# Performance work log

Measured on AMD Instinct MI355X. Metric: run time of the kernel, lower is better.

## Reference

```python
import jax, jax.numpy as jnp
import numpy as np

A, B, N, FEAT, H, R, E_PER, NACT = 3, 4096, 64, 32, 32, 6, 1536, 16


def setup_inputs() -> dict:
    key = jax.random.key(0)
    ks = jax.random.split(key, 12)
    s = 0.1
    return {
        "unary": jax.random.normal(ks[0], (A, B, N, FEAT), jnp.float32),
        "actions": jax.random.normal(ks[1], (A, B, NACT), jnp.float32),
        "w_rel": jax.random.normal(ks[2], (R, FEAT, H), jnp.float32) * s,
        "w_root": jax.random.normal(ks[3], (FEAT, H), jnp.float32) * s,
        "b_gnn": jax.random.normal(ks[4], (H,), jnp.float32) * s,
        "w1": jax.random.normal(ks[5], (A, H + NACT * (A - 1), H), jnp.float32) * s,
        "b1": jax.random.normal(ks[6], (A, H), jnp.float32) * s,
        "w2": jax.random.normal(ks[7], (A, H, NACT), jnp.float32) * s,
        "b2": jax.random.normal(ks[8], (A, NACT), jnp.float32) * s,
        "edge_src": jax.random.randint(ks[9], (E_PER,), 0, N, jnp.int32),
        "edge_dst": jax.random.randint(ks[10], (E_PER,), 0, N, jnp.int32),
        "edge_rel": jax.random.randint(ks[11], (E_PER,), 0, R, jnp.int32),
    }


def reference(unary, actions, w_rel, w_root, b_gnn, w1, b1, w2, b2,
              edge_src, edge_dst, edge_rel):
    NT = B * N  # total nodes in the batched graph
    # Replicate the shared per-graph edge list across the batch with node offsets
    offs = (jnp.arange(B, dtype=jnp.int32) * N)[:, None]
    src = (edge_src[None, :] + offs).reshape(-1)            # [E]
    dst = (edge_dst[None, :] + offs).reshape(-1)            # [E]
    rel = jnp.tile(edge_rel, B)                             # [E]
    seg = dst * R + rel                                     # per (node, relation) segment
    cnt = jax.ops.segment_sum(jnp.ones_like(rel, jnp.float32), seg,
                              num_segments=NT * R)
    inv_deg = 1.0 / jnp.maximum(cnt, 1.0)                   # RGCN mean per relation
    norm_e = inv_deg[seg][:, None]

    def rgcn_relu(x):  # x: [NT, FEAT]
        h_stack = jnp.einsum('ni,rio->rno', x, w_rel)       # [R, NT, H]
        msg = h_stack[rel, src] * norm_e                    # [E, H] gather-transform
        agg = jax.ops.segment_sum(msg, dst, num_segments=NT)
        return jax.nn.relu(agg + x @ w_root + b_gnn)

    qs = []
    for a in range(A):
        h = rgcn_relu(unary[a].reshape(NT, FEAT))           # [NT, H]
        pooled = h.reshape(B, N, H).max(axis=1)             # global max pool per graph
        others = jnp.concatenate([actions[j] for j in range(A) if j != a], axis=1)
        critic_in = jnp.concatenate([pooled, others], axis=1)
        mid = jax.nn.leaky_relu(critic_in @ w1[a] + b1[a], negative_slope=0.01)
        all_q = mid @ w2[a] + b2[a]                         # [B, NACT]
        idx = jnp.argmax(actions[a], axis=1)[:, None]
        qs.append(jnp.take_along_axis(all_q, idx, axis=1))  # [B, 1]
    return jnp.stack(qs)                                    # [A, B, 1]
```

## Files before the change

### kernel.cpp

```cpp
#include <hip/hip_runtime.h>
#include <hip/hip_bf16.h>
#include <math.h>

#define A_AG   3
#define Bq     4096
#define Nn     64
#define FEAT   32
#define Hh     32
#define Rr     6
#define E_PER  1536
#define NACT   16

#define KCAT    224
#define XSTRIDE 232
#define TSTRIDE 72
#define NDR     384
#define NEXT    448

typedef __attribute__((ext_vector_type(8))) short          bfrag;
typedef __attribute__((ext_vector_type(4))) float          f32x4;
typedef __attribute__((ext_vector_type(8))) unsigned short u16x8;

__device__ __forceinline__ ushort f2bf(float x) {
    unsigned u = __float_as_uint(x);
    u = (u + 0x7fffu + ((u >> 16) & 1u)) >> 16;
    return (ushort)u;
}
__device__ __forceinline__ float bf2f(ushort b) {
    return __uint_as_float(((unsigned)b) << 16);
}
__device__ __forceinline__ unsigned cvt_pk_bf16(float lo, float hi) {
    unsigned r;
    asm volatile("v_cvt_pk_bf16_f32 %0, %1, %2" : "=v"(r) : "v"(lo), "v"(hi));
    return r;
}

__global__ __launch_bounds__(1024) void prep(
        const float* __restrict__ w_rel,
        const float* __restrict__ w_root,
        const int* __restrict__ esrc,
        const int* __restrict__ edst,
        const int* __restrict__ erel,
        float*  __restrict__ Adjf,
        ushort* __restrict__ Adjbf,
        ushort* __restrict__ Wt_g) {
    __shared__ int   cnt[NDR];
    __shared__ float invd[NEXT];
    const int t = threadIdx.x;

    for (int i = t; i < NDR; i += 1024) cnt[i] = 0;
    __syncthreads();
    for (int e = t; e < E_PER; e += 1024)
        atomicAdd(&cnt[edst[e] * Rr + erel[e]], 1);
    __syncthreads();
    for (int i = t; i < NEXT; i += 1024)
        invd[i] = (i < NDR) ? 1.0f / fmaxf((float)cnt[i], 1.0f) : 1.0f;
    for (int i = t; i < NEXT * Nn; i += 1024) Adjf[i] = 0.f;
    __syncthreads();
    for (int e = t; e < E_PER; e += 1024)
        atomicAdd(&Adjf[(edst[e] * Rr + erel[e]) * Nn + esrc[e]], 1.0f);
    if (t < Nn) Adjf[(NDR + t) * Nn + t] = 1.0f;
    __syncthreads();
    for (int i = t; i < NEXT * Nn; i += 1024)
        Adjbf[i] = f2bf(Adjf[i] * invd[i >> 6]);
    for (int i = t; i < Hh * KCAT; i += 1024) {
        const int h = i / KCAT, kk = i % KCAT;
        float v;
        if (kk < 192) v = w_rel[(((kk >> 5) * FEAT) + (kk & 31)) * Hh + h];
        else          v = w_root[(kk - 192) * Hh + h];
        Wt_g[i] = f2bf(v);
    }
}

__global__ __launch_bounds__(256, 4) void critic_kernel(
    const float* __restrict__ unary,
    const float* __restrict__ actions,
    const float* __restrict__ b_gnn,
    const float* __restrict__ w1,
    const float* __restrict__ b1,
    const float* __restrict__ w2,
    const float* __restrict__ b2,
    const ushort* __restrict__ Adj,
    const ushort* __restrict__ Wt,
    float* __restrict__ out)
{
    const int b = blockIdx.x;
    const int a = blockIdx.y;
    const int t = threadIdx.x;

    __shared__ ushort Xt[FEAT * TSTRIDE];
    __shared__ ushort xcat[Nn * XSTRIDE];
    __shared__ float pmax[4][32];
    __shared__ float cin[64];
    __shared__ float mid[32];
    __shared__ float allq[16];

    {
        const int f = t & 31, sg = t >> 5;
        const float* xp = unary + ((((size_t)a * Bq + b) * Nn + sg * 8) * FEAT) + f;
        unsigned w0 = cvt_pk_bf16(xp[0 * FEAT], xp[1 * FEAT]);
        unsigned w1_ = cvt_pk_bf16(xp[2 * FEAT], xp[3 * FEAT]);
        unsigned w2_ = cvt_pk_bf16(xp[4 * FEAT], xp[5 * FEAT]);
        unsigned w3 = cvt_pk_bf16(xp[6 * FEAT], xp[7 * FEAT]);
        uint4 v = {w0, w1_, w2_, w3};
        *(uint4*)&Xt[f * TSTRIDE + sg * 8] = v;
    }
    __syncthreads();

    {
        const int l = t & 63, w = t >> 6;
        const int lr = l & 15, kg = l >> 4;

        bfrag af[2][2];
        #pragma unroll
        for (int mt = 0; mt < 2; ++mt)
            #pragma unroll
            for (int ks = 0; ks < 2; ++ks)
                af[mt][ks] = *(const bfrag*)&Xt[(mt * 16 + lr) * TSTRIDE + ks * 32 + kg * 8];

        const ushort* abase = Adj + (size_t)(w * 7 * 16 + lr) * Nn + kg * 8;
        f32x4 acc[7][2];
        #pragma unroll
        for (int i = 0; i < 7; ++i) {
            acc[i][0] = (f32x4){0.f, 0.f, 0.f, 0.f};
            acc[i][1] = (f32x4){0.f, 0.f, 0.f, 0.f};
        }
        #pragma unroll
        for (int i = 0; i < 7; ++i) {
            const bfrag b0 = *(const bfrag*)(abase + i * 16 * Nn);
            const bfrag b1f = *(const bfrag*)(abase + i * 16 * Nn + 32);
            acc[i][0] = __builtin_amdgcn_mfma_f32_16x16x32_bf16(af[0][0], b0,  acc[i][0], 0, 0, 0);
            acc[i][1] = __builtin_amdgcn_mfma_f32_16x16x32_bf16(af[1][0], b0,  acc[i][1], 0, 0, 0);
            acc[i][0] = __builtin_amdgcn_mfma_f32_16x16x32_bf16(af[0][1], b1f, acc[i][0], 0, 0, 0);
            acc[i][1] = __builtin_amdgcn_mfma_f32_16x16x32_bf16(af[1][1], b1f, acc[i][1], 0, 0, 0);
        }
        #pragma unroll
        for (int i = 0; i < 7; ++i) {
            const int nt = w * 7 + i;
            const int dr = nt * 16 + lr;
            int row, colb;
            if (nt < 24) {
                const int d = (dr * 10923) >> 16;
                const int r = dr - 6 * d;
                row = d; colb = r * 32;
            } else {
                row = dr - NDR; colb = 192;
            }
            #pragma unroll
            for (int mt = 0; mt < 2; ++mt) {
                const unsigned lo = cvt_pk_bf16(acc[i][mt][0], acc[i][mt][1]);
                const unsigned hi = cvt_pk_bf16(acc[i][mt][2], acc[i][mt][3]);
                uint2 v = {lo, hi};
                *(uint2*)&xcat[row * XSTRIDE + colb + mt * 16 + kg * 4] = v;
            }
        }
    }
    __syncthreads();

    {
        const int l = t & 63, w = t >> 6;
        const int lr = l & 15, kg = l >> 4;
        const ushort* arow  = &xcat[(w * 16 + lr) * XSTRIDE + kg * 8];
        const ushort* bcol0 = Wt + lr * KCAT + kg * 8;
        const ushort* bcol1 = Wt + (16 + lr) * KCAT + kg * 8;
        f32x4 acc0 = {0.f, 0.f, 0.f, 0.f};
        f32x4 acc1 = {0.f, 0.f, 0.f, 0.f};
        #pragma unroll
        for (int ks = 0; ks < 7; ++ks) {
            const bfrag afr = *(const bfrag*)(arow + ks * 32);
            const bfrag b0  = *(const bfrag*)(bcol0 + ks * 32);
            const bfrag b1  = *(const bfrag*)(bcol1 + ks * 32);
            acc0 = __builtin_amdgcn_mfma_f32_16x16x32_bf16(afr, b0, acc0, 0, 0, 0);
            acc1 = __builtin_amdgcn_mfma_f32_16x16x32_bf16(afr, b1, acc1, 0, 0, 0);
        }
        const float bg0 = b_gnn[lr], bg1 = b_gnn[16 + lr];
        float m0 = -INFINITY, m1 = -INFINITY;
        #pragma unroll
        for (int j = 0; j < 4; ++j) {
            m0 = fmaxf(m0, fmaxf(acc0[j] + bg0, 0.f));
            m1 = fmaxf(m1, fmaxf(acc1[j] + bg1, 0.f));
        }
        m0 = fmaxf(m0, __shfl_xor(m0, 16));
        m0 = fmaxf(m0, __shfl_xor(m0, 32));
        m1 = fmaxf(m1, __shfl_xor(m1, 16));
        m1 = fmaxf(m1, __shfl_xor(m1, 32));
        if (l < 16) { pmax[w][lr] = m0; pmax[w][16 + lr] = m1; }
    }
    __syncthreads();

    if (t < 32) {
        cin[t] = fmaxf(fmaxf(pmax[0][t], pmax[1][t]),
                       fmaxf(pmax[2][t], pmax[3][t]));
    } else if (t < 64) {
        const int k   = t - 32;
        const int jj  = k >> 4;
        const int col = k & 15;
        const int other = (jj == 0) ? (a == 0 ? 1 : 0) : (a == 2 ? 1 : 2);
        cin[t] = actions[((size_t)other * Bq + b) * NACT + col];
    }
    __syncthreads();

    if (t < 32) {
        float acc = b1[a * Hh + t];
        #pragma unroll
        for (int k = 0; k < 64; ++k)
            acc = fmaf(cin[k], w1[((size_t)a * 64 + k) * Hh + t], acc);
        mid[t] = acc > 0.f ? acc : 0.01f * acc;
    }
    __syncthreads();

    if (t < 16) {
        float acc = b2[a * NACT + t];
        #pragma unroll
        for (int k = 0; k < 32; ++k)
            acc = fmaf(mid[k], w2[((size_t)a * Hh + k) * NACT + t], acc);
        allq[t] = acc;
    }
    __syncthreads();

    if (t == 0) {
        const float* act = actions + ((size_t)a * Bq + b) * NACT;
        int best = 0;
        float bv = act[0];
        #pragma unroll
        for (int j = 1; j < NACT; ++j) {
            float v = act[j];
            if (v > bv) { bv = v; best = j; }
        }
        out[(size_t)a * Bq + b] = allq[best];
    }
}

extern "C" void kernel_launch(void* const* d_in, const int* in_sizes, int n_in,
                              void* d_out, int out_size, void* d_ws, size_t ws_size,
                              hipStream_t stream) {
    const float* unary   = (const float*)d_in[0];
    const float* actions = (const float*)d_in[1];
    const float* w_rel   = (const float*)d_in[2];
    const float* w_root  = (const float*)d_in[3];
    const float* b_gnn   = (const float*)d_in[4];
    const float* w1      = (const float*)d_in[5];
    const float* b1      = (const float*)d_in[6];
    const float* w2      = (const float*)d_in[7];
    const float* b2      = (const float*)d_in[8];
    const int* edge_src  = (const int*)d_in[9];
    const int* edge_dst  = (const int*)d_in[10];
    const int* edge_rel  = (const int*)d_in[11];
    float* out = (float*)d_out;

    char* ws = (char*)d_ws;
    ushort* Adjbf = (ushort*)(ws + 0);
    ushort* Wt_g  = (ushort*)(ws + 57344);
    float*  Adjf  = (float*)(ws + 71680);

    prep<<<1, 1024, 0, stream>>>(w_rel, w_root, edge_src, edge_dst, edge_rel,
                                 Adjf, Adjbf, Wt_g);

    dim3 grid(Bq, A_AG);
    critic_kernel<<<grid, 256, 0, stream>>>(unary, actions, b_gnn,
                                            w1, b1, w2, b2,
                                            Adjbf, Wt_g, out);
}
```

Measured before the change: 302.4 us.

## Split critic MLP tail into separate batched kernel over 8 graphs per block

Moves the pooled-feature MLP head (two small dense layers plus action argmax selection) out of the per-graph GNN kernel into a new tail kernel. The GNN kernel now writes pooled features to workspace, and the tail kernel processes 8 graphs per block with w1/w2 staged in shared memory. This removes serialized tail phases in which most threads sat idle behind several block-wide barriers in every GNN block. The cost is an extra kernel launch and a workspace round trip for the pooled features.

After: 289.5 us. -4.3%, faster.

```diff
diff --git a/kernel.cpp b/kernel.cpp
--- a/kernel.cpp
+++ b/kernel.cpp
@@ -16,18 +16,15 @@
 #define TSTRIDE 72
 #define NDR     384
 #define NEXT    448
+#define GT      8
 
 typedef __attribute__((ext_vector_type(8))) short          bfrag;
 typedef __attribute__((ext_vector_type(4))) float          f32x4;
-typedef __attribute__((ext_vector_type(8))) unsigned short u16x8;
 
 __device__ __forceinline__ ushort f2bf(float x) {
     unsigned u = __float_as_uint(x);
     u = (u + 0x7fffu + ((u >> 16) & 1u)) >> 16;
     return (ushort)u;
-}
-__device__ __forceinline__ float bf2f(ushort b) {
-    return __uint_as_float(((unsigned)b) << 16);
 }
 __device__ __forceinline__ unsigned cvt_pk_bf16(float lo, float hi) {
     unsigned r;
@@ -74,15 +71,10 @@
 
 __global__ __launch_bounds__(256, 4) void critic_kernel(
     const float* __restrict__ unary,
-    const float* __restrict__ actions,
     const float* __restrict__ b_gnn,
-    const float* __restrict__ w1,
-    const float* __restrict__ b1,
-    const float* __restrict__ w2,
-    const float* __restrict__ b2,
     const ushort* __restrict__ Adj,
     const ushort* __restrict__ Wt,
-    float* __restrict__ out)
+    float* __restrict__ pooled_g)
 {
     const int b = blockIdx.x;
     const int a = blockIdx.y;
@@ -91,9 +83,6 @@
     __shared__ ushort Xt[FEAT * TSTRIDE];
     __shared__ ushort xcat[Nn * XSTRIDE];
     __shared__ float pmax[4][32];
-    __shared__ float cin[64];
-    __shared__ float mid[32];
-    __shared__ float allq[16];
 
     {
         const int f = t & 31, sg = t >> 5;
@@ -127,12 +116,12 @@
         }
         #pragma unroll
         for (int i = 0; i < 7; ++i) {
-            const bfrag b0 = *(const bfrag*)(abase + i * 16 * Nn);
-            const bfrag b1f = *(const bfrag*)(abase + i * 16 * Nn + 32);
-            acc[i][0] = __builtin_amdgcn_mfma_f32_16x16x32_bf16(af[0][0], b0,  acc[i][0], 0, 0, 0);
-            acc[i][1] = __builtin_amdgcn_mfma_f32_16x16x32_bf16(af[1][0], b0,  acc[i][1], 0, 0, 0);
-            acc[i][0] = __builtin_amdgcn_mfma_f32_16x16x32_bf16(af[0][1], b1f, acc[i][0], 0, 0, 0);
-            acc[i][1] = __builtin_amdgcn_mfma_f32_16x16x32_bf16(af[1][1], b1f, acc[i][1], 0, 0, 0);
+            const bfrag bb0 = *(const bfrag*)(abase + i * 16 * Nn);
+            const bfrag bb1 = *(const bfrag*)(abase + i * 16 * Nn + 32);
+            acc[i][0] = __builtin_amdgcn_mfma_f32_16x16x32_bf16(af[0][0], bb0, acc[i][0], 0, 0, 0);
+            acc[i][1] = __builtin_amdgcn_mfma_f32_16x16x32_bf16(af[1][0], bb0, acc[i][1], 0, 0, 0);
+            acc[i][0] = __builtin_amdgcn_mfma_f32_16x16x32_bf16(af[0][1], bb1, acc[i][0], 0, 0, 0);
+            acc[i][1] = __builtin_amdgcn_mfma_f32_16x16x32_bf16(af[1][1], bb1, acc[i][1], 0, 0, 0);
         }
         #pragma unroll
         for (int i = 0; i < 7; ++i) {
@@ -168,10 +157,10 @@
         #pragma unroll
         for (int ks = 0; ks < 7; ++ks) {
             const bfrag afr = *(const bfrag*)(arow + ks * 32);
-            const bfrag b0  = *(const bfrag*)(bcol0 + ks * 32);
-            const bfrag b1  = *(const bfrag*)(bcol1 + ks * 32);
-            acc0 = __builtin_amdgcn_mfma_f32_16x16x32_bf16(afr, b0, acc0, 0, 0, 0);
-            acc1 = __builtin_amdgcn_mfma_f32_16x16x32_bf16(afr, b1, acc1, 0, 0, 0);
+            const bfrag bf0 = *(const bfrag*)(bcol0 + ks * 32);
+            const bfrag bf1 = *(const bfrag*)(bcol1 + ks * 32);
+            acc0 = __builtin_amdgcn_mfma_f32_16x16x32_bf16(afr, bf0, acc0, 0, 0, 0);
+            acc1 = __builtin_amdgcn_mfma_f32_16x16x32_bf16(afr, bf1, acc1, 0, 0, 0);
         }
         const float bg0 = b_gnn[lr], bg1 = b_gnn[16 + lr];
         float m0 = -INFINITY, m1 = -INFINITY;
@@ -189,45 +178,86 @@
     __syncthreads();
 
     if (t < 32) {
-        cin[t] = fmaxf(fmaxf(pmax[0][t], pmax[1][t]),
-                       fmaxf(pmax[2][t], pmax[3][t]));
-    } else if (t < 64) {
-        const int k   = t - 32;
-        const int jj  = k >> 4;
-        const int col = k & 15;
-        const int other = (jj == 0) ? (a == 0 ? 1 : 0) : (a == 2 ? 1 : 2);
-        cin[t] = actions[((size_t)other * Bq + b) * NACT + col];
-    }
-    __syncthreads();
-
-    if (t < 32) {
-        float acc = b1[a * Hh + t];
-        #pragma unroll
-        for (int k = 0; k < 64; ++k)
-            acc = fmaf(cin[k], w1[((size_t)a * 64 + k) * Hh + t], acc);
-        mid[t] = acc > 0.f ? acc : 0.01f * acc;
-    }
-    __syncthreads();
-
-    if (t < 16) {
-        float acc = b2[a * NACT + t];
+        const float p = fmaxf(fmaxf(pmax[0][t], pmax[1][t]),
+                              fmaxf(pmax[2][t], pmax[3][t]));
+        pooled_g[((size_t)a * Bq + b) * Hh + t] = p;
+    }
+}
+
+__global__ __launch_bounds__(256) void tail_kernel(
+    const float* __restrict__ pooled_g,
+    const float* __restrict__ actions,
+    const float* __restrict__ w1,
+    const float* __restrict__ b1,
+    const float* __restrict__ w2,
+    const float* __restrict__ b2,
+    float* __restrict__ out)
+{
+    const int b0 = blockIdx.x * GT;
+    const int a  = blockIdx.y;
+    const int t  = threadIdx.x;
+
+    __shared__ float w1s[64][32];
+    __shared__ float w2s[32][16];
+    __shared__ float b1s[32];
+    __shared__ float b2s[16];
+    __shared__ float pl[GT][32];
+    __shared__ float acts[GT][48];
+    __shared__ float mids[GT][32];
+    __shared__ float allq[GT][16];
+
+    for (int i = t; i < 64 * 32; i += 256)
+        w1s[i >> 5][i & 31] = w1[(size_t)a * 2048 + i];
+    for (int i = t; i < 32 * 16; i += 256)
+        w2s[i >> 4][i & 15] = w2[(size_t)a * 512 + i];
+    if (t < 32) b1s[t] = b1[a * Hh + t];
+    else if (t < 48) b2s[t - 32] = b2[a * NACT + (t - 32)];
+    {
+        const int g = t >> 5, h = t & 31;
+        pl[g][h] = pooled_g[((size_t)a * Bq + b0 + g) * Hh + h];
+    }
+    for (int i = t; i < GT * 48; i += 256) {
+        const int g = i / 48, j = i - g * 48;
+        int src_a, col;
+        if (j < 16)      { src_a = a;                 col = j; }
+        else if (j < 32) { src_a = (a == 0 ? 1 : 0);  col = j - 16; }
+        else             { src_a = (a == 2 ? 1 : 2);  col = j - 32; }
+        acts[g][j] = actions[((size_t)src_a * Bq + b0 + g) * NACT + col];
+    }
+    __syncthreads();
+
+    {
+        const int g = t >> 5, h = t & 31;
+        float acc = b1s[h];
         #pragma unroll
         for (int k = 0; k < 32; ++k)
-            acc = fmaf(mid[k], w2[((size_t)a * Hh + k) * NACT + t], acc);
-        allq[t] = acc;
-    }
-    __syncthreads();
-
-    if (t == 0) {
-        const float* act = actions + ((size_t)a * Bq + b) * NACT;
+            acc = fmaf(pl[g][k], w1s[k][h], acc);
+        #pragma unroll
+        for (int k = 0; k < 32; ++k)
+            acc = fmaf(acts[g][16 + k], w1s[32 + k][h], acc);
+        mids[g][h] = acc > 0.f ? acc : 0.01f * acc;
+    }
+    __syncthreads();
+
+    if (t < 128) {
+        const int g = t >> 4, q = t & 15;
+        float acc = b2s[q];
+        #pragma unroll
+        for (int k = 0; k < 32; ++k)
+            acc = fmaf(mids[g][k], w2s[k][q], acc);
+        allq[g][q] = acc;
+    }
+    __syncthreads();
+
+    if (t < GT) {
         int best = 0;
-        float bv = act[0];
+        float bv = acts[t][0];
         #pragma unroll
         for (int j = 1; j < NACT; ++j) {
-            float v = act[j];
+            const float v = acts[t][j];
             if (v > bv) { bv = v; best = j; }
         }
-        out[(size_t)a * Bq + b] = allq[best];
+        out[(size_t)a * Bq + b0 + t] = allq[t][best];
     }
 }
 
@@ -249,15 +279,17 @@
     float* out = (float*)d_out;
 
     char* ws = (char*)d_ws;
-    ushort* Adjbf = (ushort*)(ws + 0);
-    ushort* Wt_g  = (ushort*)(ws + 57344);
-    float*  Adjf  = (float*)(ws + 71680);
+    float*  pooled_g = (float*)(ws + 0);
+    ushort* Adjbf    = (ushort*)(ws + 1572864);
+    ushort* Wt_g     = (ushort*)(ws + 1630208);
+    float*  Adjf     = (float*)(ws + 1644544);
 
     prep<<<1, 1024, 0, stream>>>(w_rel, w_root, edge_src, edge_dst, edge_rel,
                                  Adjf, Adjbf, Wt_g);
 
     dim3 grid(Bq, A_AG);
-    critic_kernel<<<grid, 256, 0, stream>>>(unary, actions, b_gnn,
-                                            w1, b1, w2, b2,
-                                            Adjbf, Wt_g, out);
-}
+    critic_kernel<<<grid, 256, 0, stream>>>(unary, b_gnn, Adjbf, Wt_g, pooled_g);
+
+    dim3 tgrid(Bq / GT, A_AG);
+    tail_kernel<<<tgrid, 256, 0, stream>>>(pooled_g, actions, w1, b1, w2, b2, out);
+}
```
